# Performance work log

Measured on AMD Instinct MI355X. Metric: run time of the kernel, lower is better.

## Reference

```python
import jax, jax.numpy as jnp
import numpy as np

H = 512
V = 32000
B = 64
S = 64
T = 64
SOS = 0


def setup_inputs() -> dict:
    key = jax.random.key(0)
    ks = jax.random.split(key, 20)
    s = 1.0 / np.sqrt(H)
    return {
        "encoder_outputs": jax.random.normal(ks[0], (B, S, H), jnp.float32),
        "encoder_hidden": jax.random.normal(ks[1], (1, B, H), jnp.float32),
        "target_tensor": jax.random.randint(ks[2], (B, T), 0, V),
        "emb": jax.random.normal(ks[3], (V, H), jnp.float32) * s,
        "Wa": jax.random.normal(ks[4], (H, H), jnp.float32) * s,
        "ba": jnp.zeros((H,), jnp.float32),
        "Ua": jax.random.normal(ks[5], (H, H), jnp.float32) * s,
        "bu": jnp.zeros((H,), jnp.float32),
        "Va": jax.random.normal(ks[6], (1, H), jnp.float32) * s,
        "bv": jnp.zeros((1,), jnp.float32),
        "W_ih": jax.random.normal(ks[7], (3 * H, 2 * H), jnp.float32) * s,
        "W_hh": jax.random.normal(ks[8], (3 * H, H), jnp.float32) * s,
        "b_ih": jnp.zeros((3 * H,), jnp.float32),
        "b_hh": jnp.zeros((3 * H,), jnp.float32),
        "W_out": jax.random.normal(ks[9], (V, H), jnp.float32) * s,
        "b_out": jnp.zeros((V,), jnp.float32),
    }


def reference(encoder_outputs, encoder_hidden, target_tensor, emb, Wa, ba, Ua, bu,
              Va, bv, W_ih, W_hh, b_ih, b_hh, W_out, b_out):
    # Teacher-forced inputs: SOS then target[:, :-1]
    sos = jnp.full((B, 1), SOS, dtype=target_tensor.dtype)
    inputs = jnp.concatenate([sos, target_tensor[:, :-1]], axis=1)  # [B,T]
    emb_seq = emb[inputs]  # [B,T,H]

    # Precompute Ua(keys): invariant across decode steps
    Uk = jnp.einsum('bsh,kh->bsk', encoder_outputs, Ua) + bu  # [B,S,H]
    h0 = encoder_hidden[0]  # [B,H]

    def step(h, x_t):
        # Bahdanau attention: Va * tanh(Wa q + Ua k)
        q = h @ Wa.T + ba                                   # [B,H]
        scores = jnp.tanh(q[:, None, :] + Uk) @ Va[0] + bv[0]  # [B,S]
        w = jax.nn.softmax(scores, axis=-1)                 # [B,S]
        ctx = jnp.einsum('bs,bsh->bh', w, encoder_outputs)  # [B,H]
        # GRU cell (PyTorch gate layout: r, z, n)
        x = jnp.concatenate([x_t, ctx], axis=-1)            # [B,2H]
        gi = x @ W_ih.T + b_ih
        gh = h @ W_hh.T + b_hh
        ir, iz, inn = jnp.split(gi, 3, axis=-1)
        hr, hz, hn = jnp.split(gh, 3, axis=-1)
        r = jax.nn.sigmoid(ir + hr)
        z = jax.nn.sigmoid(iz + hz)
        n = jnp.tanh(inn + r * hn)
        h_new = (1.0 - z) * n + z * h
        logits = h_new @ W_out.T + b_out                    # [B,V]
        return h_new, (logits, w)

    hT, (logits, attn) = jax.lax.scan(step, h0, jnp.swapaxes(emb_seq, 0, 1))
    log_probs = jax.nn.log_softmax(jnp.swapaxes(logits, 0, 1), axis=-1)  # [B,T,V]
    attentions = jnp.swapaxes(attn, 0, 1)                                # [B,T,S]
    return log_probs, hT[None], attentions
```

## Files before the change

kernel.cpp:

```cpp
#include <hip/hip_runtime.h>
#include <math.h>

#define HH 512
#define VV 32000
#define BB 64
#define SS 64
#define TT 64
#define H3 1536

#define WS_GIEMBBF 0LL
#define WS_UKBF    3145728LL
#define WS_ENCBF   4194304LL
#define WS_EMBBF   5242880LL
#define WS_WCATBF  6291456LL
#define WS_WIHC3   6815744LL
#define WS_WIHE    7208960LL
#define WS_UABF    7602176LL
#define WS_WHH3    7733248LL
#define WS_BCAT    8126464LL
#define WS_CTXBF   8128512LL
#define WS_H32     8144896LL
#define WS_HBF     8210432LL
#define WS_HSALL   8388608LL

#define OUT_HT  ((long long)BB*TT*VV)
#define OUT_ATT (OUT_HT + (long long)BB*HH)

typedef __attribute__((ext_vector_type(8))) short bf16x8;
typedef __attribute__((ext_vector_type(4))) float f32x4;

__device__ inline unsigned short f2b(float x) {
  unsigned u = __builtin_bit_cast(unsigned, x);
  unsigned r = (u + 0x7FFF + ((u >> 16) & 1)) >> 16;
  return (unsigned short)r;
}
__device__ inline float bc(unsigned u) { return __builtin_bit_cast(float, u); }
__device__ inline float b2f(unsigned short h) { return bc(((unsigned)h) << 16); }
__device__ inline float frcp(float x) { return __builtin_amdgcn_rcpf(x); }
__device__ inline float tanh_fast(float x) { return 1.f - 2.f * frcp(__expf(2.f * x) + 1.f); }
__device__ inline float sigm(float x) { return frcp(1.f + __expf(-x)); }

#define GLDS(gp, lp) __builtin_amdgcn_global_load_lds( \
    (const __attribute__((address_space(1))) void*)(gp), \
    (__attribute__((address_space(3))) void*)(lp), 16, 0, 0)

__global__ __launch_bounds__(256) void build_wcat_kernel(const float* __restrict__ Wa,
    const float* __restrict__ Whh, const float* __restrict__ ba,
    const float* __restrict__ bhh, unsigned short* __restrict__ wcatbf,
    float* __restrict__ bcat)
{
  long long i = (long long)blockIdx.x * 256 + threadIdx.x;
  int j = (int)(i >> 9), k = (int)(i & 511);
  float v = (j < HH) ? Wa[(long long)j*HH + k] : Whh[(long long)(j - HH)*HH + k];
  wcatbf[i] = f2b(v);
  if (i < 2048) bcat[i] = (i < HH) ? ba[i] : bhh[i - HH];
}

__global__ __launch_bounds__(256) void build_g3_kernel(const float* __restrict__ Wsrc,
    unsigned short* __restrict__ o, int ld, int ofs)
{
  long long i = (long long)blockIdx.x * 256 + threadIdx.x;
  int rp = (int)(i >> 9), k = (int)(i & 511);
  int j = rp / 3, g = rp - j * 3;
  o[i] = f2b(Wsrc[((long long)(g*512 + j))*ld + ofs + k]);
}

__global__ __launch_bounds__(256) void build_wihe_kernel(const float* __restrict__ W_ih,
    unsigned short* __restrict__ o)
{
  long long i = (long long)blockIdx.x * 256 + threadIdx.x;
  o[i] = f2b(W_ih[(long long)(i >> 9)*1024 + (i & 511)]);
}

__global__ __launch_bounds__(256) void cvt_f2b_kernel(const float* __restrict__ in,
    unsigned short* __restrict__ outp, long long n)
{
  long long i = ((long long)blockIdx.x * 256 + threadIdx.x) * 4;
  if (i >= n) return;
  float4 v = *(const float4*)(in + i);
  ushort4 r = { f2b(v.x), f2b(v.y), f2b(v.z), f2b(v.w) };
  *(ushort4*)(outp + i) = r;
}

__global__ __launch_bounds__(256) void build_embbf_kernel(const float* __restrict__ emb,
    const int* __restrict__ tgt, unsigned short* __restrict__ embbf)
{
  const int m = blockIdx.x, t = m >> 6, b = m & 63;
  const int tk = (t == 0) ? 0 : tgt[b*TT + t - 1];
  const float* src = emb + (long long)tk*HH;
  unsigned short* dst = embbf + (long long)m*HH;
  const int i = threadIdx.x;
  dst[i] = f2b(src[i]);
  dst[i + 256] = f2b(src[i + 256]);
}

__global__ __launch_bounds__(256) void hinit_kernel(const float* __restrict__ eh,
    unsigned short* __restrict__ hbf0, float* __restrict__ h320)
{
  int i = blockIdx.x * 256 + threadIdx.x;
  float v = eh[i];
  hbf0[i] = f2b(v);
  h320[i] = v;
}

template<int OUTBF>
__global__ __launch_bounds__(256) void mfma_nt(const unsigned short* __restrict__ A,
    const unsigned short* __restrict__ Bw, const float* __restrict__ bias,
    void* __restrict__ Cv, long long ldc)
{
  __shared__ unsigned short As[128*32];
  __shared__ unsigned short Bs[128*32];
  const int tid = threadIdx.x;
  const int w = tid >> 6, l = tid & 63;
  const int m0 = blockIdx.y * 128, n0 = blockIdx.x * 128;
  const int wr = w >> 1, wc = w & 1;

  f32x4 acc[4][4];
  #pragma unroll
  for (int i = 0; i < 4; i++)
    #pragma unroll
    for (int j = 0; j < 4; j++) acc[i][j] = (f32x4){0.f, 0.f, 0.f, 0.f};

  const int srow = l >> 2;
  const int scol = (l & 3) * 8;

  for (int k0 = 0; k0 < HH; k0 += 32) {
    __syncthreads();
    #pragma unroll
    for (int q = 0; q < 2; ++q) {
      int r = w*32 + q*16 + srow;
      GLDS(A  + (long long)(m0 + r)*HH + k0 + scol, As + r*32 + scol);
      GLDS(Bw + (long long)(n0 + r)*HH + k0 + scol, Bs + r*32 + scol);
    }
    __syncthreads();

    bf16x8 a[4], b[4];
    #pragma unroll
    for (int mi = 0; mi < 4; mi++)
      a[mi] = *(const bf16x8*)&As[(wr*64 + mi*16 + (l & 15))*32 + (l >> 4)*8];
    #pragma unroll
    for (int ni = 0; ni < 4; ni++)
      b[ni] = *(const bf16x8*)&Bs[(wc*64 + ni*16 + (l & 15))*32 + (l >> 4)*8];
    #pragma unroll
    for (int mi = 0; mi < 4; mi++)
      #pragma unroll
      for (int ni = 0; ni < 4; ni++)
        acc[mi][ni] = __builtin_amdgcn_mfma_f32_16x16x32_bf16(a[mi], b[ni], acc[mi][ni], 0, 0, 0);
  }

  #pragma unroll
  for (int mi = 0; mi < 4; mi++) {
    #pragma unroll
    for (int ni = 0; ni < 4; ni++) {
      int col = n0 + wc*64 + ni*16 + (l & 15);
      float bb = bias[col];
      #pragma unroll
      for (int r2 = 0; r2 < 4; r2++) {
        int row = m0 + wr*64 + mi*16 + (l >> 4)*4 + r2;
        float v = acc[mi][ni][r2] + bb;
        if (OUTBF) ((unsigned short*)Cv)[(long long)row*ldc + col] = f2b(v);
        else       ((float*)Cv)[(long long)row*ldc + col] = v;
      }
    }
  }
}

__global__ __launch_bounds__(256) void q_attn_kernel(int t,
    const unsigned short* __restrict__ hbf_r, const unsigned short* __restrict__ wabf,
    const float* __restrict__ bcat, const unsigned short* __restrict__ ukbf,
    const unsigned short* __restrict__ encbf, const float* __restrict__ Va,
    const float* __restrict__ bvp,
    unsigned short* __restrict__ ctxbf, float* __restrict__ attn_out)
{
  const int b = blockIdx.x, tid = threadIdx.x;
  const int w = tid >> 6, l = tid & 63;
  __shared__ unsigned short hsh[512];
  __shared__ unsigned short Ws[512*32];
  __shared__ float qs2[8][68];
  __shared__ float vsh[8][68];
  __shared__ float sc[SS], sw[SS];

  ((unsigned*)hsh)[tid] = ((const unsigned*)(hbf_r + (long long)b*512))[tid];
  vsh[tid >> 6][tid & 63] = Va[tid];
  vsh[(tid + 256) >> 6][tid & 63] = Va[tid + 256];
  __syncthreads();

  f32x4 acc[8];
  #pragma unroll
  for (int i = 0; i < 8; i++) acc[i] = (f32x4){0.f, 0.f, 0.f, 0.f};

  for (int k0 = 0; k0 < HH; k0 += 32) {
    if (k0) __syncthreads();
    #pragma unroll
    for (int q = 0; q < 8; ++q) {
      int idx = tid + q*256;
      int r = idx >> 2, c8 = (idx & 3) * 8;
      GLDS(wabf + (long long)r*HH + k0 + c8, Ws + r*32 + c8);
    }
    __syncthreads();

    bf16x8 a = *(const bf16x8*)&hsh[k0 + (l >> 4)*8];
    #pragma unroll
    for (int i = 0; i < 8; ++i) {
      bf16x8 bfr = *(const bf16x8*)&Ws[(w*128 + i*16 + (l & 15))*32 + (l >> 4)*8];
      acc[i] = __builtin_amdgcn_mfma_f32_16x16x32_bf16(a, bfr, acc[i], 0, 0, 0);
    }
  }
  if (l < 16) {
    #pragma unroll
    for (int i = 0; i < 8; ++i) {
      int col = w*128 + i*16 + l;
      qs2[col >> 6][col & 63] = acc[i][0] + bcat[col];
    }
  }
  __syncthreads();

  {
    const int s = tid >> 2, sub = tid & 3;
    float p_ = 0.f;
    #pragma unroll
    for (int half = 0; half < 2; ++half) {
      const int row = sub*2 + half;
      const uint4* up = (const uint4*)(ukbf + ((long long)(b*SS + s))*512 + row*64);
      const float* qp = &qs2[row][0];
      const float* vp = &vsh[row][0];
      #pragma unroll
      for (int i = 0; i < 8; ++i) {
        uint4 uv = up[i];
        int e = i*8;
        p_ = fmaf(vp[e+0], tanh_fast(qp[e+0] + bc(uv.x << 16)), p_);
        p_ = fmaf(vp[e+1], tanh_fast(qp[e+1] + bc(uv.x & 0xffff0000u)), p_);
        p_ = fmaf(vp[e+2], tanh_fast(qp[e+2] + bc(uv.y << 16)), p_);
        p_ = fmaf(vp[e+3], tanh_fast(qp[e+3] + bc(uv.y & 0xffff0000u)), p_);
        p_ = fmaf(vp[e+4], tanh_fast(qp[e+4] + bc(uv.z << 16)), p_);
        p_ = fmaf(vp[e+5], tanh_fast(qp[e+5] + bc(uv.z & 0xffff0000u)), p_);
        p_ = fmaf(vp[e+6], tanh_fast(qp[e+6] + bc(uv.w << 16)), p_);
        p_ = fmaf(vp[e+7], tanh_fast(qp[e+7] + bc(uv.w & 0xffff0000u)), p_);
      }
    }
    p_ += __shfl_xor(p_, 1);
    p_ += __shfl_xor(p_, 2);
    if (sub == 0) sc[s] = p_ + bvp[0];
  }
  __syncthreads();

  if (tid < 64) {
    float x = sc[tid], mx = x;
    #pragma unroll
    for (int off = 32; off; off >>= 1) mx = fmaxf(mx, __shfl_xor(mx, off));
    float e = __expf(x - mx), sm = e;
    #pragma unroll
    for (int off = 32; off; off >>= 1) sm += __shfl_xor(sm, off);
    float w_ = e * frcp(sm);
    sw[tid] = w_;
    attn_out[((long long)b*TT + t)*SS + tid] = w_;
  }
  __syncthreads();

  {
    float a0 = 0.f, a1 = 0.f;
    const unsigned short* ep = encbf + (long long)b*SS*512;
    #pragma unroll 8
    for (int s = 0; s < SS; ++s) {
      float w_ = sw[s];
      a0 = fmaf(w_, b2f(ep[s*512 + tid]), a0);
      a1 = fmaf(w_, b2f(ep[s*512 + tid + 256]), a1);
    }
    ctxbf[b*512 + tid]       = f2b(a0);
    ctxbf[b*512 + tid + 256] = f2b(a1);
  }
}

__global__ __launch_bounds__(256) void ghgic_gates_mfma(int t,
    const unsigned short* __restrict__ hbf_r, const unsigned short* __restrict__ ctxbf,
    const unsigned short* __restrict__ wihc3bf, const unsigned short* __restrict__ whh3bf,
    const float* __restrict__ bcat, const unsigned short* __restrict__ giembbf,
    const float* __restrict__ h32_r, float* __restrict__ h32_w,
    unsigned short* __restrict__ hbf_w, unsigned short* __restrict__ hsall,
    float* __restrict__ out_ht)
{
  __shared__ unsigned short As[64*32];
  __shared__ unsigned short Hs[64*32];
  __shared__ unsigned short Bs[96*32];
  __shared__ unsigned short Cs[96*32];
  __shared__ float gl[64*100];
  __shared__ float hl[64*100];
  const int tid = threadIdx.x;
  const int w = tid >> 6, l = tid & 63;
  const int n0 = blockIdx.x * 96, j0 = blockIdx.x * 32;
  const int wr = w >> 1, wc = w & 1;

  f32x4 accg[2][3], acch[2][3];
  #pragma unroll
  for (int i = 0; i < 2; i++)
    #pragma unroll
    for (int j = 0; j < 3; j++) {
      accg[i][j] = (f32x4){0.f, 0.f, 0.f, 0.f};
      acch[i][j] = (f32x4){0.f, 0.f, 0.f, 0.f};
    }

  for (int k0 = 0; k0 < HH; k0 += 32) {
    __syncthreads();
    #pragma unroll
    for (int q = 0; q < 5; ++q) {
      int idx = tid + q*256;
      if (idx < 256) {
        int r = idx >> 2, c8 = (idx & 3) * 8;
        GLDS(ctxbf + (long long)r*HH + k0 + c8, As + r*32 + c8);
      } else if (idx < 512) {
        int i2 = idx - 256, r = i2 >> 2, c8 = (i2 & 3) * 8;
        GLDS(hbf_r + (long long)r*HH + k0 + c8, Hs + r*32 + c8);
      } else if (idx < 896) {
        int i2 = idx - 512, r = i2 >> 2, c8 = (i2 & 3) * 8;
        GLDS(wihc3bf + (long long)(n0 + r)*HH + k0 + c8, Bs + r*32 + c8);
      } else {
        int i2 = idx - 896, r = i2 >> 2, c8 = (i2 & 3) * 8;
        GLDS(whh3bf + (long long)(n0 + r)*HH + k0 + c8, Cs + r*32 + c8);
      }
    }
    __syncthreads();

    bf16x8 ag[2], ah[2], bg[3], bh[3];
    #pragma unroll
    for (int mi = 0; mi < 2; mi++) {
      ag[mi] = *(const bf16x8*)&As[(wr*32 + mi*16 + (l & 15))*32 + (l >> 4)*8];
      ah[mi] = *(const bf16x8*)&Hs[(wr*32 + mi*16 + (l & 15))*32 + (l >> 4)*8];
    }
    #pragma unroll
    for (int ni = 0; ni < 3; ni++) {
      bg[ni] = *(const bf16x8*)&Bs[(wc*48 + ni*16 + (l & 15))*32 + (l >> 4)*8];
      bh[ni] = *(const bf16x8*)&Cs[(wc*48 + ni*16 + (l & 15))*32 + (l >> 4)*8];
    }
    #pragma unroll
    for (int mi = 0; mi < 2; mi++)
      #pragma unroll
      for (int ni = 0; ni < 3; ni++) {
        accg[mi][ni] = __builtin_amdgcn_mfma_f32_16x16x32_bf16(ag[mi], bg[ni], accg[mi][ni], 0, 0, 0);
        acch[mi][ni] = __builtin_amdgcn_mfma_f32_16x16x32_bf16(ah[mi], bh[ni], acch[mi][ni], 0, 0, 0);
      }
  }

  #pragma unroll
  for (int mi = 0; mi < 2; mi++)
    #pragma unroll
    for (int ni = 0; ni < 3; ni++) {
      int col = wc*48 + ni*16 + (l & 15);
      #pragma unroll
      for (int r2 = 0; r2 < 4; r2++) {
        int row = wr*32 + mi*16 + (l >> 4)*4 + r2;
        gl[row*100 + col] = accg[mi][ni][r2];
        hl[row*100 + col] = acch[mi][ni][r2];
      }
    }
  __syncthreads();

  for (int i = tid; i < 2048; i += 256) {
    const int b = i >> 5, jj = i & 31, j = j0 + jj;
    float gcr = gl[b*100 + jj*3 + 0];
    float gcz = gl[b*100 + jj*3 + 1];
    float gcn = gl[b*100 + jj*3 + 2];
    float ghr = hl[b*100 + jj*3 + 0] + bcat[512 + j];
    float ghz = hl[b*100 + jj*3 + 1] + bcat[1024 + j];
    float ghn = hl[b*100 + jj*3 + 2] + bcat[1536 + j];
    const long long gb = ((long long)t*BB + b)*H3 + j;
    float gir = b2f(giembbf[gb]);
    float giz = b2f(giembbf[gb + 512]);
    float gin = b2f(giembbf[gb + 1024]);
    float r = sigm(gir + gcr + ghr);
    float z = sigm(giz + gcz + ghz);
    float n = tanh_fast(gin + gcn + r * ghn);
    float hold = h32_r[b*512 + j];
    float hn = (1.f - z) * n + z * hold;
    h32_w[b*512 + j] = hn;
    unsigned short hb = f2b(hn);
    hbf_w[b*512 + j] = hb;
    hsall[((long long)b*TT + t)*512 + j] = hb;
    if (t == TT - 1) out_ht[b*512 + j] = hn;
  }
}

__global__ __launch_bounds__(1024) void logsoftmax_kernel(float* __restrict__ lp)
{
  float4* p4 = (float4*)(lp + (long long)blockIdx.x * VV);
  const int tid = threadIdx.x;
  float m = -1e30f, s = 0.f;
  for (int v = tid; v < 8000; v += 1024) {
    float4 x = p4[v];
    float mx = fmaxf(fmaxf(x.x, x.y), fmaxf(x.z, x.w));
    float e = __expf(x.x - mx) + __expf(x.y - mx) + __expf(x.z - mx) + __expf(x.w - mx);
    if (mx > m) { s = s * __expf(m - mx) + e; m = mx; }
    else        { s += e * __expf(mx - m); }
  }
  #pragma unroll
  for (int off = 32; off; off >>= 1) {
    float m2 = __shfl_xor(m, off), s2 = __shfl_xor(s, off);
    float mm = fmaxf(m, m2);
    s = s * __expf(m - mm) + s2 * __expf(m2 - mm);
    m = mm;
  }
  __shared__ float rm[16], rs[16];
  if ((tid & 63) == 0) { rm[tid >> 6] = m; rs[tid >> 6] = s; }
  __syncthreads();
  float M = rm[0], S = rs[0];
  #pragma unroll
  for (int i = 1; i < 16; ++i) {
    float m2 = rm[i], s2 = rs[i];
    float mm = fmaxf(M, m2);
    S = S * __expf(M - mm) + s2 * __expf(m2 - mm);
    M = mm;
  }
  const float L = M + logf(S);
  for (int v = tid; v < 8000; v += 1024) {
    float4 x = p4[v];
    x.x -= L; x.y -= L; x.z -= L; x.w -= L;
    p4[v] = x;
  }
}

extern "C" void kernel_launch(void* const* d_in, const int* in_sizes, int n_in,
                              void* d_out, int out_size, void* d_ws, size_t ws_size,
                              hipStream_t stream)
{
  const float* enc   = (const float*)d_in[0];
  const float* eh    = (const float*)d_in[1];
  const int*   tgt   = (const int*)  d_in[2];
  const float* emb   = (const float*)d_in[3];
  const float* Wa    = (const float*)d_in[4];
  const float* ba    = (const float*)d_in[5];
  const float* Ua    = (const float*)d_in[6];
  const float* bu    = (const float*)d_in[7];
  const float* Va    = (const float*)d_in[8];
  const float* bvp   = (const float*)d_in[9];
  const float* W_ih  = (const float*)d_in[10];
  const float* W_hh  = (const float*)d_in[11];
  const float* b_ih  = (const float*)d_in[12];
  const float* b_hh  = (const float*)d_in[13];
  const float* W_out = (const float*)d_in[14];
  const float* b_out = (const float*)d_in[15];

  float* out = (float*)d_out;
  float* ws  = (float*)d_ws;

  unsigned short* giembbf = (unsigned short*)(ws + WS_GIEMBBF);
  unsigned short* ukbf    = (unsigned short*)(ws + WS_UKBF);
  unsigned short* encbf   = (unsigned short*)(ws + WS_ENCBF);
  unsigned short* embbf   = (unsigned short*)(ws + WS_EMBBF);
  unsigned short* wcatbf  = (unsigned short*)(ws + WS_WCATBF);
  unsigned short* wihc3bf = (unsigned short*)(ws + WS_WIHC3);
  unsigned short* wihebf  = (unsigned short*)(ws + WS_WIHE);
  unsigned short* uabf    = (unsigned short*)(ws + WS_UABF);
  unsigned short* whh3bf  = (unsigned short*)(ws + WS_WHH3);
  float* bcat = ws + WS_BCAT;
  unsigned short* ctxbf = (unsigned short*)(ws + WS_CTXBF);
  float* h320 = ws + WS_H32;
  float* h321 = h320 + BB*HH;
  unsigned short* hbf0 = (unsigned short*)(ws + WS_HBF);
  unsigned short* hbf1 = hbf0 + BB*HH;
  unsigned short* hsall = (unsigned short*)(ws + WS_HSALL);
  unsigned short* wbf   = (unsigned short*)ws;

  float* attn_out = out + OUT_ATT;
  float* out_ht   = out + OUT_HT;

  build_wcat_kernel<<<dim3(4096), dim3(256), 0, stream>>>(Wa, W_hh, ba, b_hh, wcatbf, bcat);
  build_g3_kernel<<<dim3(3072), dim3(256), 0, stream>>>(W_ih, wihc3bf, 1024, 512);
  build_g3_kernel<<<dim3(3072), dim3(256), 0, stream>>>(W_hh, whh3bf, 512, 0);
  build_wihe_kernel<<<dim3(3072), dim3(256), 0, stream>>>(W_ih, wihebf);
  cvt_f2b_kernel<<<dim3(256), dim3(256), 0, stream>>>(Ua, uabf, (long long)HH*HH);
  cvt_f2b_kernel<<<dim3(2048), dim3(256), 0, stream>>>(enc, encbf, (long long)BB*SS*HH);
  build_embbf_kernel<<<dim3(4096), dim3(256), 0, stream>>>(emb, tgt, embbf);
  hinit_kernel<<<dim3(128), dim3(256), 0, stream>>>(eh, hbf0, h320);

  mfma_nt<1><<<dim3(4, 32), dim3(256), 0, stream>>>(encbf, uabf, bu, (void*)ukbf, (long long)HH);
  mfma_nt<1><<<dim3(12, 32), dim3(256), 0, stream>>>(embbf, wihebf, b_ih, (void*)giembbf, (long long)H3);

  for (int t = 0; t < TT; ++t) {
    const unsigned short* hr  = (t & 1) ? hbf1 : hbf0;
    const float*          h32r = (t & 1) ? h321 : h320;
    unsigned short*       hw  = (t & 1) ? hbf0 : hbf1;
    float*                h32w = (t & 1) ? h320 : h321;
    q_attn_kernel<<<dim3(64), dim3(256), 0, stream>>>(t, hr, wcatbf, bcat,
        ukbf, encbf, Va, bvp, ctxbf, attn_out);
    ghgic_gates_mfma<<<dim3(16), dim3(256), 0, stream>>>(t, hr, ctxbf, wihc3bf, whh3bf,
        bcat, giembbf, h32r, h32w, hw, hsall, out_ht);
  }

  cvt_f2b_kernel<<<dim3(16000), dim3(256), 0, stream>>>(W_out, wbf, (long long)VV*HH);
  mfma_nt<0><<<dim3(250, 32), dim3(256), 0, stream>>>(hsall, wbf, b_out, (void*)out, (long long)VV);
  logsoftmax_kernel<<<dim3(4096), dim3(1024), 0, stream>>>(out);
}
```

Before: 2.564 ms.

## Move attention query GEMM into gates kernel as split-K partials

The query projection h@Wa^T used to be recomputed redundantly by each of 64 attention blocks, each streaming all of Wa from memory. Now each gates block multiplies its 32-column slice of the new hidden state by the matching Wa slice and writes a K-partial. The attention kernel sums 16 partials plus the bias and uses 512 threads for the score and context loops. A separate qinit kernel handles step zero. This removes repeated Wa traffic and MFMA work from the serial per-step chain, at the cost of extra shared memory and partial-sum global writes and reads in the gates kernel.

```diff
diff --git a/kernel.cpp b/kernel.cpp
--- a/kernel.cpp
+++ b/kernel.cpp
@@ -18,10 +18,12 @@
 #define WS_UABF    7602176LL
 #define WS_WHH3    7733248LL
 #define WS_BCAT    8126464LL
-#define WS_CTXBF   8128512LL
-#define WS_H32     8144896LL
-#define WS_HBF     8210432LL
-#define WS_HSALL   8388608LL
+#define WS_QBUF    8128512LL
+#define WS_QPART   8161280LL
+#define WS_CTXBF   8685568LL
+#define WS_H32     8701952LL
+#define WS_HBF     8767488LL
+#define WS_HSALL   8800256LL
 
 #define OUT_HT  ((long long)BB*TT*VV)
 #define OUT_ATT (OUT_HT + (long long)BB*HH)
@@ -165,81 +167,113 @@
   }
 }
 
-__global__ __launch_bounds__(256) void q_attn_kernel(int t,
+__global__ __launch_bounds__(256) void qinit_mfma(
     const unsigned short* __restrict__ hbf_r, const unsigned short* __restrict__ wabf,
+    float* __restrict__ qbuf)
+{
+  __shared__ unsigned short As[64*32];
+  __shared__ unsigned short Bs[128*32];
+  const int tid = threadIdx.x;
+  const int w = tid >> 6, l = tid & 63;
+  const int n0 = blockIdx.x * 128;
+  const int wr = w >> 1, wc = w & 1;
+
+  f32x4 acc[2][4];
+  #pragma unroll
+  for (int i = 0; i < 2; i++)
+    #pragma unroll
+    for (int j = 0; j < 4; j++) acc[i][j] = (f32x4){0.f, 0.f, 0.f, 0.f};
+
+  const int ar = tid >> 2;
+  const int ac8 = (tid & 3) * 8;
+
+  for (int k0 = 0; k0 < HH; k0 += 32) {
+    __syncthreads();
+    GLDS(hbf_r + (long long)ar*HH + k0 + ac8, As + ar*32 + ac8);
+    #pragma unroll
+    for (int q = 0; q < 2; ++q) {
+      int r = q*64 + ar;
+      GLDS(wabf + (long long)(n0 + r)*HH + k0 + ac8, Bs + r*32 + ac8);
+    }
+    __syncthreads();
+
+    bf16x8 a[2], b[4];
+    #pragma unroll
+    for (int mi = 0; mi < 2; mi++)
+      a[mi] = *(const bf16x8*)&As[(wr*32 + mi*16 + (l & 15))*32 + (l >> 4)*8];
+    #pragma unroll
+    for (int ni = 0; ni < 4; ni++)
+      b[ni] = *(const bf16x8*)&Bs[(wc*64 + ni*16 + (l & 15))*32 + (l >> 4)*8];
+    #pragma unroll
+    for (int mi = 0; mi < 2; mi++)
+      #pragma unroll
+      for (int ni = 0; ni < 4; ni++)
+        acc[mi][ni] = __builtin_amdgcn_mfma_f32_16x16x32_bf16(a[mi], b[ni], acc[mi][ni], 0, 0, 0);
+  }
+
+  #pragma unroll
+  for (int mi = 0; mi < 2; mi++) {
+    #pragma unroll
+    for (int ni = 0; ni < 4; ni++) {
+      int col = n0 + wc*64 + ni*16 + (l & 15);
+      #pragma unroll
+      for (int r2 = 0; r2 < 4; r2++) {
+        int row = wr*32 + mi*16 + (l >> 4)*4 + r2;
+        qbuf[(long long)row*512 + col] = acc[mi][ni][r2];
+      }
+    }
+  }
+}
+
+__global__ __launch_bounds__(512) void attn_kernel(int t, int first,
+    const float* __restrict__ qbuf, const float* __restrict__ qPart,
     const float* __restrict__ bcat, const unsigned short* __restrict__ ukbf,
     const unsigned short* __restrict__ encbf, const float* __restrict__ Va,
     const float* __restrict__ bvp,
     unsigned short* __restrict__ ctxbf, float* __restrict__ attn_out)
 {
   const int b = blockIdx.x, tid = threadIdx.x;
-  const int w = tid >> 6, l = tid & 63;
-  __shared__ unsigned short hsh[512];
-  __shared__ unsigned short Ws[512*32];
   __shared__ float qs2[8][68];
   __shared__ float vsh[8][68];
   __shared__ float sc[SS], sw[SS];
 
-  ((unsigned*)hsh)[tid] = ((const unsigned*)(hbf_r + (long long)b*512))[tid];
-  vsh[tid >> 6][tid & 63] = Va[tid];
-  vsh[(tid + 256) >> 6][tid & 63] = Va[tid + 256];
+  {
+    const int c = tid;
+    float q = bcat[c];
+    if (first) {
+      q += qbuf[(long long)b*512 + c];
+    } else {
+      #pragma unroll
+      for (int i = 0; i < 16; ++i)
+        q += qPart[(long long)i*32768 + b*512 + c];
+    }
+    qs2[c >> 6][c & 63] = q;
+    vsh[c >> 6][c & 63] = Va[c];
+  }
   __syncthreads();
 
-  f32x4 acc[8];
-  #pragma unroll
-  for (int i = 0; i < 8; i++) acc[i] = (f32x4){0.f, 0.f, 0.f, 0.f};
-
-  for (int k0 = 0; k0 < HH; k0 += 32) {
-    if (k0) __syncthreads();
-    #pragma unroll
-    for (int q = 0; q < 8; ++q) {
-      int idx = tid + q*256;
-      int r = idx >> 2, c8 = (idx & 3) * 8;
-      GLDS(wabf + (long long)r*HH + k0 + c8, Ws + r*32 + c8);
-    }
-    __syncthreads();
-
-    bf16x8 a = *(const bf16x8*)&hsh[k0 + (l >> 4)*8];
+  {
+    const int s = tid >> 3, sub = tid & 7;
+    const uint4* up = (const uint4*)(ukbf + ((long long)(b*SS + s))*512 + sub*64);
+    const float* qp = &qs2[sub][0];
+    const float* vp = &vsh[sub][0];
+    float p_ = 0.f;
     #pragma unroll
     for (int i = 0; i < 8; ++i) {
-      bf16x8 bfr = *(const bf16x8*)&Ws[(w*128 + i*16 + (l & 15))*32 + (l >> 4)*8];
-      acc[i] = __builtin_amdgcn_mfma_f32_16x16x32_bf16(a, bfr, acc[i], 0, 0, 0);
-    }
-  }
-  if (l < 16) {
-    #pragma unroll
-    for (int i = 0; i < 8; ++i) {
-      int col = w*128 + i*16 + l;
-      qs2[col >> 6][col & 63] = acc[i][0] + bcat[col];
-    }
-  }
-  __syncthreads();
-
-  {
-    const int s = tid >> 2, sub = tid & 3;
-    float p_ = 0.f;
-    #pragma unroll
-    for (int half = 0; half < 2; ++half) {
-      const int row = sub*2 + half;
-      const uint4* up = (const uint4*)(ukbf + ((long long)(b*SS + s))*512 + row*64);
-      const float* qp = &qs2[row][0];
-      const float* vp = &vsh[row][0];
-      #pragma unroll
-      for (int i = 0; i < 8; ++i) {
-        uint4 uv = up[i];
-        int e = i*8;
-        p_ = fmaf(vp[e+0], tanh_fast(qp[e+0] + bc(uv.x << 16)), p_);
-        p_ = fmaf(vp[e+1], tanh_fast(qp[e+1] + bc(uv.x & 0xffff0000u)), p_);
-        p_ = fmaf(vp[e+2], tanh_fast(qp[e+2] + bc(uv.y << 16)), p_);
-        p_ = fmaf(vp[e+3], tanh_fast(qp[e+3] + bc(uv.y & 0xffff0000u)), p_);
-        p_ = fmaf(vp[e+4], tanh_fast(qp[e+4] + bc(uv.z << 16)), p_);
-        p_ = fmaf(vp[e+5], tanh_fast(qp[e+5] + bc(uv.z & 0xffff0000u)), p_);
-        p_ = fmaf(vp[e+6], tanh_fast(qp[e+6] + bc(uv.w << 16)), p_);
-        p_ = fmaf(vp[e+7], tanh_fast(qp[e+7] + bc(uv.w & 0xffff0000u)), p_);
-      }
+      uint4 uv = up[i];
+      int e = i*8;
+      p_ = fmaf(vp[e+0], tanh_fast(qp[e+0] + bc(uv.x << 16)), p_);
+      p_ = fmaf(vp[e+1], tanh_fast(qp[e+1] + bc(uv.x & 0xffff0000u)), p_);
+      p_ = fmaf(vp[e+2], tanh_fast(qp[e+2] + bc(uv.y << 16)), p_);
+      p_ = fmaf(vp[e+3], tanh_fast(qp[e+3] + bc(uv.y & 0xffff0000u)), p_);
+      p_ = fmaf(vp[e+4], tanh_fast(qp[e+4] + bc(uv.z << 16)), p_);
+      p_ = fmaf(vp[e+5], tanh_fast(qp[e+5] + bc(uv.z & 0xffff0000u)), p_);
+      p_ = fmaf(vp[e+6], tanh_fast(qp[e+6] + bc(uv.w << 16)), p_);
+      p_ = fmaf(vp[e+7], tanh_fast(qp[e+7] + bc(uv.w & 0xffff0000u)), p_);
     }
     p_ += __shfl_xor(p_, 1);
     p_ += __shfl_xor(p_, 2);
+    p_ += __shfl_xor(p_, 4);
     if (sub == 0) sc[s] = p_ + bvp[0];
   }
   __syncthreads();
@@ -258,31 +292,30 @@
   __syncthreads();
 
   {
-    float a0 = 0.f, a1 = 0.f;
-    const unsigned short* ep = encbf + (long long)b*SS*512;
+    float a = 0.f;
+    const unsigned short* ep = encbf + (long long)b*SS*512 + tid;
     #pragma unroll 8
-    for (int s = 0; s < SS; ++s) {
-      float w_ = sw[s];
-      a0 = fmaf(w_, b2f(ep[s*512 + tid]), a0);
-      a1 = fmaf(w_, b2f(ep[s*512 + tid + 256]), a1);
-    }
-    ctxbf[b*512 + tid]       = f2b(a0);
-    ctxbf[b*512 + tid + 256] = f2b(a1);
-  }
-}
-
-__global__ __launch_bounds__(256) void ghgic_gates_mfma(int t,
+    for (int s = 0; s < SS; ++s)
+      a = fmaf(sw[s], b2f(ep[s*512]), a);
+    ctxbf[b*512 + tid] = f2b(a);
+  }
+}
+
+__global__ __launch_bounds__(256) void gates_qgh_mfma(int t, int last,
     const unsigned short* __restrict__ hbf_r, const unsigned short* __restrict__ ctxbf,
     const unsigned short* __restrict__ wihc3bf, const unsigned short* __restrict__ whh3bf,
-    const float* __restrict__ bcat, const unsigned short* __restrict__ giembbf,
+    const unsigned short* __restrict__ wabf, const float* __restrict__ bcat,
+    const unsigned short* __restrict__ giembbf,
     const float* __restrict__ h32_r, float* __restrict__ h32_w,
     unsigned short* __restrict__ hbf_w, unsigned short* __restrict__ hsall,
-    float* __restrict__ out_ht)
+    float* __restrict__ out_ht, float* __restrict__ qPart)
 {
   __shared__ unsigned short As[64*32];
   __shared__ unsigned short Hs[64*32];
   __shared__ unsigned short Bs[96*32];
   __shared__ unsigned short Cs[96*32];
+  __shared__ unsigned short Was[512*32];
+  __shared__ unsigned short hnewp[64*40];
   __shared__ float gl[64*100];
   __shared__ float hl[64*100];
   const int tid = threadIdx.x;
@@ -338,6 +371,15 @@
         accg[mi][ni] = __builtin_amdgcn_mfma_f32_16x16x32_bf16(ag[mi], bg[ni], accg[mi][ni], 0, 0, 0);
         acch[mi][ni] = __builtin_amdgcn_mfma_f32_16x16x32_bf16(ah[mi], bh[ni], acch[mi][ni], 0, 0, 0);
       }
+  }
+
+  if (!last) {
+    #pragma unroll
+    for (int q = 0; q < 8; ++q) {
+      int idx = tid + q*256;
+      int r = idx >> 2, c8 = (idx & 3) * 8;
+      GLDS(wabf + (long long)r*HH + j0 + c8, Was + r*32 + c8);
+    }
   }
 
   #pragma unroll
@@ -375,7 +417,42 @@
     unsigned short hb = f2b(hn);
     hbf_w[b*512 + j] = hb;
     hsall[((long long)b*TT + t)*512 + j] = hb;
+    hnewp[b*40 + jj] = hb;
     if (t == TT - 1) out_ht[b*512 + j] = hn;
+  }
+  __syncthreads();
+
+  if (!last) {
+    f32x4 qa[4][8];
+    #pragma unroll
+    for (int mi = 0; mi < 4; mi++)
+      #pragma unroll
+      for (int ni = 0; ni < 8; ni++) qa[mi][ni] = (f32x4){0.f, 0.f, 0.f, 0.f};
+
+    bf16x8 a[4];
+    #pragma unroll
+    for (int mi = 0; mi < 4; mi++)
+      a[mi] = *(const bf16x8*)&hnewp[(mi*16 + (l & 15))*40 + (l >> 4)*8];
+    #pragma unroll
+    for (int ni = 0; ni < 8; ni++) {
+      bf16x8 bfr = *(const bf16x8*)&Was[(w*128 + ni*16 + (l & 15))*32 + (l >> 4)*8];
+      #pragma unroll
+      for (int mi = 0; mi < 4; mi++)
+        qa[mi][ni] = __builtin_amdgcn_mfma_f32_16x16x32_bf16(a[mi], bfr, qa[mi][ni], 0, 0, 0);
+    }
+
+    float* qp = qPart + (long long)blockIdx.x * 32768;
+    #pragma unroll
+    for (int mi = 0; mi < 4; mi++)
+      #pragma unroll
+      for (int ni = 0; ni < 8; ni++) {
+        int col = w*128 + ni*16 + (l & 15);
+        #pragma unroll
+        for (int r2 = 0; r2 < 4; r2++) {
+          int row = mi*16 + (l >> 4)*4 + r2;
+          qp[row*512 + col] = qa[mi][ni][r2];
+        }
+      }
   }
 }
 
@@ -450,7 +527,9 @@
   unsigned short* wihebf  = (unsigned short*)(ws + WS_WIHE);
   unsigned short* uabf    = (unsigned short*)(ws + WS_UABF);
   unsigned short* whh3bf  = (unsigned short*)(ws + WS_WHH3);
-  float* bcat = ws + WS_BCAT;
+  float* bcat  = ws + WS_BCAT;
+  float* qbuf  = ws + WS_QBUF;
+  float* qPart = ws + WS_QPART;
   unsigned short* ctxbf = (unsigned short*)(ws + WS_CTXBF);
   float* h320 = ws + WS_H32;
   float* h321 = h320 + BB*HH;
@@ -474,15 +553,18 @@
   mfma_nt<1><<<dim3(4, 32), dim3(256), 0, stream>>>(encbf, uabf, bu, (void*)ukbf, (long long)HH);
   mfma_nt<1><<<dim3(12, 32), dim3(256), 0, stream>>>(embbf, wihebf, b_ih, (void*)giembbf, (long long)H3);
 
+  qinit_mfma<<<dim3(4), dim3(256), 0, stream>>>(hbf0, wcatbf, qbuf);
+
   for (int t = 0; t < TT; ++t) {
     const unsigned short* hr  = (t & 1) ? hbf1 : hbf0;
     const float*          h32r = (t & 1) ? h321 : h320;
     unsigned short*       hw  = (t & 1) ? hbf0 : hbf1;
     float*                h32w = (t & 1) ? h320 : h321;
-    q_attn_kernel<<<dim3(64), dim3(256), 0, stream>>>(t, hr, wcatbf, bcat,
-        ukbf, encbf, Va, bvp, ctxbf, attn_out);
-    ghgic_gates_mfma<<<dim3(16), dim3(256), 0, stream>>>(t, hr, ctxbf, wihc3bf, whh3bf,
-        bcat, giembbf, h32r, h32w, hw, hsall, out_ht);
+    attn_kernel<<<dim3(64), dim3(512), 0, stream>>>(t, (t == 0) ? 1 : 0, qbuf, qPart,
+        bcat, ukbf, encbf, Va, bvp, ctxbf, attn_out);
+    gates_qgh_mfma<<<dim3(16), dim3(256), 0, stream>>>(t, (t == TT - 1) ? 1 : 0,
+        hr, ctxbf, wihc3bf, whh3bf, wcatbf, bcat, giembbf,
+        h32r, h32w, hw, hsall, out_ht, qPart);
   }
 
   cvt_f2b_kernel<<<dim3(16000), dim3(256), 0, stream>>>(W_out, wbf, (long long)VV*HH);
```

New measurement: 2.183 ms. 1.17x faster.
